# Optimization experiments

Hardware: AMD Instinct MI355X
Metric: run time of the kernel (lower is better)

Reference implementation:

```python
import jax, jax.numpy as jnp
import numpy as np

W_WORKERS = 2
Q_LEN = 16
HIDDEN = 4096
N_HEADS = 32
N_KV = 8
HEAD_DIM = 128
L_SHARED = 8192
L_WORKER = 2048
THETA = 10000.0


def rotate_half(x):
    x1, x2 = jnp.split(x, 2, axis=-1)
    return jnp.concatenate((-x2, x1), axis=-1)


def rope_cos_sin(pos):
    # pos: int array [...]; returns cos,sin of shape [..., HEAD_DIM] (HF convention: freqs duplicated)
    inv = 1.0 / (THETA ** (jnp.arange(0, HEAD_DIM, 2, dtype=jnp.float32) / HEAD_DIM))
    ang = pos[..., None].astype(jnp.float32) * inv
    emb = jnp.concatenate((ang, ang), axis=-1)
    return jnp.cos(emb), jnp.sin(emb)


def setup_inputs() -> dict:
    key = jax.random.key(0)
    ks = jax.random.split(key, 16)
    std = 0.02
    # new keys are appended at positions L_WORKER..L_WORKER+Q-1 of each worker's own segment
    pos_new = jnp.broadcast_to(L_WORKER + jnp.arange(Q_LEN), (W_WORKERS, Q_LEN))
    cos_new, sin_new = rope_cos_sin(pos_new)
    return {
        'hidden_states': jax.random.normal(ks[0], (W_WORKERS, Q_LEN, HIDDEN), jnp.float32),
        'Wq': jax.random.normal(ks[1], (N_HEADS * HEAD_DIM, HIDDEN), jnp.float32) * std,
        'bq': jnp.zeros((N_HEADS * HEAD_DIM,), jnp.float32),
        'Wk': jax.random.normal(ks[2], (N_KV * HEAD_DIM, HIDDEN), jnp.float32) * std,
        'bk': jnp.zeros((N_KV * HEAD_DIM,), jnp.float32),
        'Wv': jax.random.normal(ks[3], (N_KV * HEAD_DIM, HIDDEN), jnp.float32) * std,
        'bv': jnp.zeros((N_KV * HEAD_DIM,), jnp.float32),
        'Wo': jax.random.normal(ks[4], (HIDDEN, N_HEADS * HEAD_DIM), jnp.float32) * std,
        'seg_shared_k': jax.random.normal(ks[5], (N_KV, L_SHARED, HEAD_DIM), jnp.float32),
        'seg_shared_v': jax.random.normal(ks[6], (N_KV, L_SHARED, HEAD_DIM), jnp.float32),
        'w0_k': jax.random.normal(ks[7], (N_KV, L_WORKER, HEAD_DIM), jnp.float32),
        'w0_v': jax.random.normal(ks[8], (N_KV, L_WORKER, HEAD_DIM), jnp.float32),
        'w1_k': jax.random.normal(ks[9], (N_KV, L_WORKER, HEAD_DIM), jnp.float32),
        'w1_v': jax.random.normal(ks[10], (N_KV, L_WORKER, HEAD_DIM), jnp.float32),
        'cos_new': cos_new,
        'sin_new': sin_new,
    }


def reference(hidden_states, Wq, bq, Wk, bk, Wv, bv, Wo,
              seg_shared_k, seg_shared_v, w0_k, w0_v, w1_k, w1_v,
              cos_new, sin_new):
    W, Q, _ = hidden_states.shape
    scale = HEAD_DIM ** -0.5
    # projections -> [W, n_heads, Q, D]
    q = (hidden_states @ Wq.T + bq).reshape(W, Q, N_HEADS, HEAD_DIM).transpose(0, 2, 1, 3)
    k_new = (hidden_states @ Wk.T + bk).reshape(W, Q, N_KV, HEAD_DIM).transpose(0, 2, 1, 3)
    v_new = (hidden_states @ Wv.T + bv).reshape(W, Q, N_KV, HEAD_DIM).transpose(0, 2, 1, 3)
    # rope new keys (unsqueeze_dim=1: broadcast over kv heads)
    c, s = cos_new[:, None], sin_new[:, None]
    k_new = k_new * c + rotate_half(k_new) * s
    # cache update: segment 0 = shared prompt, segment 1/2 = worker 0/1 own cache (grows by Q)
    keys = [seg_shared_k,
            jnp.concatenate([w0_k, k_new[0]], axis=1),
            jnp.concatenate([w1_k, k_new[1]], axis=1)]
    values = [seg_shared_v,
              jnp.concatenate([w0_v, v_new[0]], axis=1),
              jnp.concatenate([w1_v, v_new[1]], axis=1)]
    frag_lens = [L_SHARED, L_WORKER + Q, L_WORKER + Q]
    # worker w's view: [shared, other worker's cache, own cache]
    orders = [[0, 2, 1], [0, 1, 2]]
    loc = np.zeros((3, W_WORKERS, Q), dtype=np.int32)
    for w, order in enumerate(orders):
        pos = 0
        for seg in reversed(order):
            pos += frag_lens[seg]
            loc[seg, w] = np.arange(pos - Q, pos)
    loc = jnp.asarray(loc)  # [S, W, Q]
    cos_q, sin_q = rope_cos_sin(loc)  # [S, W, Q, D]
    # hogwild_rope: queries rotated per (segment, worker) location -> [S, W, H, Q, D]
    rq = q[None] * cos_q[:, :, None] + rotate_half(q)[None] * sin_q[:, :, None]
    rep = N_HEADS // N_KV
    scores, v_parts = [], []
    for seg in range(3):
        k_s = jnp.repeat(keys[seg], rep, axis=0)  # GQA expand [H, L_s, D]
        sc = jnp.einsum('whqd,hld->whql', rq[seg], k_s) * scale
        mask = jnp.arange(frag_lens[seg])[None, None, None, :] <= loc[seg][:, None, :, None]
        scores.append(jnp.where(mask, sc, jnp.finfo(sc.dtype).min))
        v_parts.append(jnp.repeat(values[seg], rep, axis=0))
    scores = jnp.concatenate(scores, axis=-1)        # [W, H, Q, Ltot] joint softmax over fragments
    probs = jax.nn.softmax(scores, axis=-1)
    v_all = jnp.concatenate(v_parts, axis=1)         # [H, Ltot, D]
    attn = jnp.einsum('whql,hld->whqd', probs, v_all)
    out = attn.transpose(0, 2, 1, 3).reshape(W, Q, N_HEADS * HEAD_DIM) @ Wo.T
    return out
```

## Files before the change

### kernel.cpp

```cpp
#include <hip/hip_runtime.h>
#include <hip/hip_fp16.h>
#include <cstdint>
#include <cstddef>

#define QL 16
#define LSH 8192
#define LWK 2048
#define SCALE 0.08838834764831845f

typedef __attribute__((ext_vector_type(8))) short short8;
typedef __attribute__((ext_vector_type(4))) float f32x4;
typedef __attribute__((ext_vector_type(8))) unsigned short ushort8v;

__device__ __forceinline__ unsigned short f2bf(float f) {
  unsigned int u = __float_as_uint(f);
  u += 0x7fffu + ((u >> 16) & 1u);
  return (unsigned short)(u >> 16);
}
__device__ __forceinline__ float bf2f(unsigned short b) {
  return __uint_as_float(((unsigned int)b) << 16);
}

__global__ __launch_bounds__(256) void k_cast(
    const float* __restrict__ in, unsigned short* __restrict__ outp, int n4)
{
  int i = blockIdx.x * 256 + threadIdx.x;
  if (i < n4) {
    float4 v = ((const float4*)in)[i];
    ushort4 p; p.x = f2bf(v.x); p.y = f2bf(v.y); p.z = f2bf(v.z); p.w = f2bf(v.w);
    ((ushort4*)outp)[i] = p;
  }
}

__global__ __launch_bounds__(512) void k_gemm3(
    const unsigned short* __restrict__ Xbf,
    const float* __restrict__ W0, const float* __restrict__ W1, const float* __restrict__ W2,
    const float* __restrict__ b0, const float* __restrict__ b1, const float* __restrict__ b2,
    float* __restrict__ out, int Ntot)
{
  __shared__ float Red[8][512];
  const int n0 = blockIdx.x * 16;
  const float* W; const float* bias; int row0;
  if (n0 < 4096)      { W = W0; bias = b0; row0 = n0; }
  else if (n0 < 5120) { W = W1; bias = b1; row0 = n0 - 4096; }
  else                { W = W2; bias = b2; row0 = n0 - 5120; }
  const int t = threadIdx.x;
  const int w_id = t >> 6;
  const int lane = t & 63;
  const int l15 = lane & 15;
  const int quad = lane >> 4;
  const int kbase = w_id * 512;

  const float* wp = W + (size_t)(row0 + l15) * 4096 + kbase + quad * 8;
  const unsigned short* xp0 = Xbf + (size_t)l15 * 4096 + kbase + quad * 8;
  const unsigned short* xp1 = xp0 + (size_t)16 * 4096;

  f32x4 C0 = {0.f,0.f,0.f,0.f}, C1 = {0.f,0.f,0.f,0.f};

  float4 wa = *(const float4*)(wp);
  float4 wb = *(const float4*)(wp + 4);
  short8 a0 = *(const short8*)(xp0);
  short8 a1 = *(const short8*)(xp1);

#pragma unroll
  for (int s = 0; s < 16; ++s) {
    float4 nwa, nwb; short8 na0, na1;
    if (s < 15) {
      nwa = *(const float4*)(wp + (s + 1) * 32);
      nwb = *(const float4*)(wp + (s + 1) * 32 + 4);
      na0 = *(const short8*)(xp0 + (s + 1) * 32);
      na1 = *(const short8*)(xp1 + (s + 1) * 32);
    }
    short8 bfr;
    bfr[0] = (short)f2bf(wa.x); bfr[1] = (short)f2bf(wa.y);
    bfr[2] = (short)f2bf(wa.z); bfr[3] = (short)f2bf(wa.w);
    bfr[4] = (short)f2bf(wb.x); bfr[5] = (short)f2bf(wb.y);
    bfr[6] = (short)f2bf(wb.z); bfr[7] = (short)f2bf(wb.w);
    C0 = __builtin_amdgcn_mfma_f32_16x16x32_bf16(a0, bfr, C0, 0, 0, 0);
    C1 = __builtin_amdgcn_mfma_f32_16x16x32_bf16(a1, bfr, C1, 0, 0, 0);
    wa = nwa; wb = nwb; a0 = na0; a1 = na1;
  }
#pragma unroll
  for (int i = 0; i < 4; ++i) {
    Red[w_id][(quad * 4 + i) * 16 + l15] = C0[i];
    Red[w_id][(16 + quad * 4 + i) * 16 + l15] = C1[i];
  }
  __syncthreads();
  {
    int m = t >> 4, n = t & 15;
    float s = 0.f;
#pragma unroll
    for (int w = 0; w < 8; ++w) s += Red[w][t];
    if (bias) s += bias[row0 + n];
    out[(size_t)m * Ntot + n0 + n] = s;
  }
}

__global__ __launch_bounds__(256) void k_rope(
    const float* __restrict__ qkv,
    const float* __restrict__ cosn, const float* __restrict__ sinn,
    unsigned short* __restrict__ rq, unsigned short* __restrict__ knew,
    unsigned short* __restrict__ vnew)
{
  const int g = blockIdx.x * 256 + threadIdx.x;
  const float LOGTH = 9.210340371976184f;
  if (g < 393216) {
    int d = g & 127, q = (g >> 7) & 15, head = (g >> 11) & 31, w = (g >> 16) & 1, var = g >> 17;
    int tok = w * 16 + q;
    int col = head * 128 + d;
    float val = qkv[(size_t)tok * 6144 + col];
    float rot = (d < 64) ? -qkv[(size_t)tok * 6144 + col + 64]
                         :  qkv[(size_t)tok * 6144 + col - 64];
    int pos = (var == 0 ? 12304 : (var == 1 ? 4112 : 2048)) + q;
    int i = d & 63;
    float inv = expf(-(float)i * (LOGTH / 64.0f));
    float ang = (float)pos * inv;
    float c = cosf(ang), s = sinf(ang);
    rq[g] = f2bf((val * c + rot * s) * SCALE);
  } else {
    int g2 = g - 393216;
    if (g2 < 65536) {
      int isv = (g2 >= 32768);
      if (isv) g2 -= 32768;
      int d = g2 & 127, q = (g2 >> 7) & 15, h = (g2 >> 11) & 7, w = (g2 >> 14) & 1;
      int tok = w * 16 + q;
      if (isv) {
        vnew[g2] = f2bf(qkv[(size_t)tok * 6144 + 5120 + h * 128 + d]);
      } else {
        int col = 4096 + h * 128 + d;
        float val = qkv[(size_t)tok * 6144 + col];
        float rot = (d < 64) ? -qkv[(size_t)tok * 6144 + col + 64]
                             :  qkv[(size_t)tok * 6144 + col - 64];
        float c = cosn[tok * 128 + d], s = sinn[tok * 128 + d];
        knew[g2] = f2bf(val * c + rot * s);
      }
    }
  }
}

__global__ __launch_bounds__(256, 2) void k_attn(
    const float* __restrict__ shk, const float* __restrict__ shv,
    const float* __restrict__ w0k, const float* __restrict__ w0v,
    const float* __restrict__ w1k, const float* __restrict__ w1v,
    const unsigned short* __restrict__ rq,
    const unsigned short* __restrict__ knew, const unsigned short* __restrict__ vnew,
    __half* __restrict__ accP, float* __restrict__ lP)
{
  __shared__ alignas(16) unsigned short Ks[64 * 136];
  __shared__ alignas(16) unsigned short Vts[128 * 72];
  __shared__ alignas(16) unsigned short Plds[4 * 32 * 72];

  const int h = blockIdx.x / 50;
  const int cidx = blockIdx.x % 50;
  int kind, k0, nk; bool is_new;
  if (cidx < 32)      { kind = 0; k0 = cidx * 256; nk = 256; is_new = false; }
  else if (cidx < 41) { int c = cidx - 32; kind = 1; k0 = c * 256; nk = (c == 8) ? 16 : 256; is_new = (c == 8); }
  else                { int c = cidx - 41; kind = 2; k0 = c * 256; nk = (c == 8) ? 16 : 256; is_new = (c == 8); }

  const int t = threadIdx.x;
  const int w_id = t >> 6;
  const int lane = t & 63;
  const int l15 = lane & 15;
  const int quad = lane >> 4;
  const int worker = w_id >> 1;
  const int headpair = w_id & 1;
  const int tg = t >> 7;
  const int dv = t & 127;
  const int rbase = t >> 5;
  const int doff = (t & 31) * 4;

  int var; bool causal;
  if (kind == 0)      { var = 0; causal = false; }
  else if (kind == 1) { var = (worker == 0) ? 2 : 1; causal = (worker == 0); }
  else                { var = (worker == 1) ? 2 : 1; causal = (worker == 1); }

  const float* Ksrc = (kind == 0) ? (shk + (size_t)h * LSH * 128)
                     : (kind == 1) ? (w0k + (size_t)h * LWK * 128)
                                   : (w1k + (size_t)h * LWK * 128);
  const float* Vsrc = (kind == 0) ? (shv + (size_t)h * LSH * 128)
                     : (kind == 1) ? (w0v + (size_t)h * LWK * 128)
                                   : (w1v + (size_t)h * LWK * 128);
  const int wseg = (kind == 2) ? 1 : 0;
  const unsigned short* knsrc = knew + ((size_t)wseg * 8 + h) * 16 * 128;
  const unsigned short* vnsrc = vnew + ((size_t)wseg * 8 + h) * 16 * 128;

  short8 arq[2][4];
#pragma unroll
  for (int mt = 0; mt < 2; ++mt) {
    int head = h * 4 + headpair * 2 + mt;
    const unsigned short* base =
        rq + ((((size_t)var * 2 + worker) * 32 + head) * 16 + l15) * 128 + quad * 8;
#pragma unroll
    for (int ks = 0; ks < 4; ++ks) arq[mt][ks] = *(const short8*)(base + ks * 32);
  }

  float lrow[2][4];
  f32x4 acc[2][8];
#pragma unroll
  for (int mt = 0; mt < 2; ++mt)
#pragma unroll
    for (int i = 0; i < 4; ++i) lrow[mt][i] = 0.0f;
#pragma unroll
  for (int mt = 0; mt < 2; ++mt)
#pragma unroll
    for (int dt = 0; dt < 8; ++dt) acc[mt][dt] = {0.f,0.f,0.f,0.f};

  float4 kf[8];
  float  vf[32];

  auto load_tile = [&](int st) {
    const int kb = k0 + st * 64;
    if (!is_new) {
#pragma unroll
      for (int rd = 0; rd < 8; ++rd)
        kf[rd] = *(const float4*)(Ksrc + (size_t)(kb + rd * 8 + rbase) * 128 + doff);
#pragma unroll
      for (int g = 0; g < 4; ++g)
#pragma unroll
        for (int i = 0; i < 8; ++i)
          vf[g * 8 + i] = Vsrc[(size_t)(kb + (tg + g * 2) * 8 + i) * 128 + dv];
    } else {
#pragma unroll
      for (int rd = 0; rd < 8; ++rd) {
        ushort4 p = *(const ushort4*)(knsrc + (size_t)((rd * 8 + rbase) & 15) * 128 + doff);
        kf[rd].x = bf2f(p.x); kf[rd].y = bf2f(p.y);
        kf[rd].z = bf2f(p.z); kf[rd].w = bf2f(p.w);
      }
#pragma unroll
      for (int g = 0; g < 4; ++g)
#pragma unroll
        for (int i = 0; i < 8; ++i)
          vf[g * 8 + i] = bf2f(vnsrc[(size_t)(((tg + g * 2) * 8 + i) & 15) * 128 + dv]);
    }
  };

  const int nst = (nk + 63) >> 6;
  load_tile(0);

  for (int st = 0; st < nst; ++st) {
    __syncthreads();
#pragma unroll
    for (int rd = 0; rd < 8; ++rd) {
      ushort4 p; p.x = f2bf(kf[rd].x); p.y = f2bf(kf[rd].y);
      p.z = f2bf(kf[rd].z); p.w = f2bf(kf[rd].w);
      *(ushort4*)(&Ks[(rd * 8 + rbase) * 136 + doff]) = p;
    }
#pragma unroll
    for (int g = 0; g < 4; ++g) {
      ushort8v p;
#pragma unroll
      for (int i = 0; i < 8; ++i) p[i] = f2bf(vf[g * 8 + i]);
      *(ushort8v*)(&Vts[dv * 72 + (tg + g * 2) * 8]) = p;
    }
    __syncthreads();
    if (st + 1 < nst) load_tile(st + 1);

#pragma unroll
    for (int mt = 0; mt < 2; ++mt) {
      f32x4 S[4];
#pragma unroll
      for (int nt = 0; nt < 4; ++nt) S[nt] = {0.f,0.f,0.f,0.f};
#pragma unroll
      for (int ks = 0; ks < 4; ++ks)
#pragma unroll
        for (int nt = 0; nt < 4; ++nt) {
          short8 bfr = *(const short8*)(&Ks[(nt * 16 + l15) * 136 + ks * 32 + quad * 8]);
          S[nt] = __builtin_amdgcn_mfma_f32_16x16x32_bf16(arq[mt][ks], bfr, S[nt], 0, 0, 0);
        }
      if (is_new) {
#pragma unroll
        for (int nt = 0; nt < 4; ++nt) {
          int loc = st * 64 + nt * 16 + l15;
          bool kval = (loc < nk);
#pragma unroll
          for (int i = 0; i < 4; ++i)
            if (!kval || (causal && loc > (quad * 4 + i))) S[nt][i] = -3.0e38f;
        }
      }
      float rs[4] = {0.f, 0.f, 0.f, 0.f};
#pragma unroll
      for (int nt = 0; nt < 4; ++nt)
#pragma unroll
        for (int i = 0; i < 4; ++i) {
          float p = expf(fminf(S[nt][i], 60.0f));
          S[nt][i] = p;
          rs[i] += p;
        }
#pragma unroll
      for (int nt = 0; nt < 4; ++nt)
#pragma unroll
        for (int i = 0; i < 4; ++i)
          Plds[w_id * (32 * 72) + (mt * 16 + quad * 4 + i) * 72 + nt * 16 + l15] =
              f2bf(S[nt][i]);
#pragma unroll
      for (int off = 1; off < 16; off <<= 1)
#pragma unroll
        for (int i = 0; i < 4; ++i) rs[i] += __shfl_xor(rs[i], off, 64);
#pragma unroll
      for (int i = 0; i < 4; ++i) lrow[mt][i] += rs[i];
    }
    short8 ap[2][2];
#pragma unroll
    for (int mt = 0; mt < 2; ++mt)
#pragma unroll
      for (int ks2 = 0; ks2 < 2; ++ks2)
        ap[mt][ks2] = *(const short8*)(
            &Plds[w_id * (32 * 72) + (mt * 16 + l15) * 72 + ks2 * 32 + quad * 8]);
#pragma unroll
    for (int dt = 0; dt < 8; ++dt)
#pragma unroll
      for (int ks2 = 0; ks2 < 2; ++ks2) {
        short8 bfr = *(const short8*)(&Vts[(dt * 16 + l15) * 72 + ks2 * 32 + quad * 8]);
        acc[0][dt] = __builtin_amdgcn_mfma_f32_16x16x32_bf16(ap[0][ks2], bfr, acc[0][dt], 0, 0, 0);
        acc[1][dt] = __builtin_amdgcn_mfma_f32_16x16x32_bf16(ap[1][ks2], bfr, acc[1][dt], 0, 0, 0);
      }
  }

  __half* accB = accP + (size_t)blockIdx.x * 128 * 128;
#pragma unroll
  for (int mt = 0; mt < 2; ++mt)
#pragma unroll
    for (int dt = 0; dt < 8; ++dt)
#pragma unroll
      for (int i = 0; i < 4; ++i) {
        int row = w_id * 32 + mt * 16 + quad * 4 + i;
        int d = dt * 16 + l15;
        accB[row * 128 + d] = __float2half(acc[mt][dt][i]);
      }
  if (l15 == 0) {
#pragma unroll
    for (int mt = 0; mt < 2; ++mt)
#pragma unroll
      for (int i = 0; i < 4; ++i) {
        int row = w_id * 32 + mt * 16 + quad * 4 + i;
        lP[(size_t)blockIdx.x * 128 + row] = lrow[mt][i];
      }
  }
}

__global__ __launch_bounds__(128) void k_combine(
    const __half* __restrict__ accP, const float* __restrict__ lP,
    unsigned short* __restrict__ attnX)
{
  __shared__ float sl[50];
  const int h = blockIdx.x >> 7;
  const int r = blockIdx.x & 127;
  const int d = threadIdx.x;
  if (d < 50) sl[d] = lP[(size_t)(h * 50 + d) * 128 + r];
  __syncthreads();
  float L = 0.0f, A = 0.0f;
#pragma unroll
  for (int c = 0; c < 50; ++c) L += sl[c];
#pragma unroll
  for (int cc = 0; cc < 50; cc += 10) {
    float p[10];
#pragma unroll
    for (int i = 0; i < 10; ++i)
      p[i] = __half2float(accP[((size_t)(h * 50 + cc + i) * 128 + r) * 128 + d]);
#pragma unroll
    for (int i = 0; i < 10; ++i) A += p[i];
  }
  int workerv = r >> 6, headpairv = (r >> 5) & 1, mtv = (r >> 4) & 1, q = r & 15;
  int head = h * 4 + headpairv * 2 + mtv;
  attnX[(size_t)(workerv * 16 + q) * 4096 + head * 128 + d] = f2bf(A / L);
}

extern "C" void kernel_launch(void* const* d_in, const int* in_sizes, int n_in,
                              void* d_out, int out_size, void* d_ws, size_t ws_size,
                              hipStream_t stream)
{
  const float* hs   = (const float*)d_in[0];
  const float* Wq   = (const float*)d_in[1];
  const float* bq   = (const float*)d_in[2];
  const float* Wk   = (const float*)d_in[3];
  const float* bk   = (const float*)d_in[4];
  const float* Wv   = (const float*)d_in[5];
  const float* bv   = (const float*)d_in[6];
  const float* Wo   = (const float*)d_in[7];
  const float* shk  = (const float*)d_in[8];
  const float* shv  = (const float*)d_in[9];
  const float* w0k  = (const float*)d_in[10];
  const float* w0v  = (const float*)d_in[11];
  const float* w1k  = (const float*)d_in[12];
  const float* w1v  = (const float*)d_in[13];
  const float* cosn = (const float*)d_in[14];
  const float* sinn = (const float*)d_in[15];
  float* out = (float*)d_out;

  char* ws = (char*)d_ws;
  float*          qkv    = (float*)(ws + 0);
  unsigned short* rq     = (unsigned short*)(ws + 786432);
  unsigned short* knew   = (unsigned short*)(ws + 1572864);
  unsigned short* vnew   = (unsigned short*)(ws + 1638400);
  unsigned short* hsbf   = (unsigned short*)(ws + 1703936);
  unsigned short* attnXb = (unsigned short*)(ws + 1966080);
  float*          lP     = (float*)(ws + 2228224);
  __half*         accP   = (__half*)(ws + 2433024);

  k_cast<<<128, 256, 0, stream>>>(hs, hsbf, 32768);
  k_gemm3<<<384, 512, 0, stream>>>(hsbf, Wq, Wk, Wv, bq, bk, bv, qkv, 6144);
  k_rope<<<1792, 256, 0, stream>>>(qkv, cosn, sinn, rq, knew, vnew);
  k_attn<<<400, 256, 0, stream>>>(shk, shv, w0k, w0v, w1k, w1v, rq, knew, vnew, accP, lP);
  k_combine<<<1024, 128, 0, stream>>>(accP, lP, attnXb);
  k_gemm3<<<256, 512, 0, stream>>>(attnXb, Wo, Wo, Wo, nullptr, nullptr, nullptr, out, 4096);
}
```

Before: 308.0 us.

## Split-K GEMMs with LDS-staged weights and keep attention probabilities in registers

The QKV and output projection GEMMs are restructured into a split-K form. Each block handles half of K and stages its fp32 weight rows into LDS with global_load_lds, then writes a partial result. A separate add kernel, or the rope kernel for QKV, sums the two partials. Attention now computes S transposed (K as the A operand), so each lane's probabilities can feed a 16x16x16 bf16 MFMA directly, with no LDS round-trip and a cheaper row-sum reduction. The cost is an extra kernel launch, extra partial-sum traffic, and reliance on the mfma 16x16x16 builtin being available.

```diff
diff --git a/kernel.cpp b/kernel.cpp
--- a/kernel.cpp
+++ b/kernel.cpp
@@ -9,8 +9,15 @@
 #define SCALE 0.08838834764831845f
 
 typedef __attribute__((ext_vector_type(8))) short short8;
+typedef __attribute__((ext_vector_type(4))) short short4v;
 typedef __attribute__((ext_vector_type(4))) float f32x4;
 typedef __attribute__((ext_vector_type(8))) unsigned short ushort8v;
+
+#if defined(__has_builtin)
+#if __has_builtin(__builtin_amdgcn_mfma_f32_16x16x16bf16_1k)
+#define HAVE_MFMA16 1
+#endif
+#endif
 
 __device__ __forceinline__ unsigned short f2bf(float f) {
   unsigned int u = __float_as_uint(f);
@@ -19,6 +26,12 @@
 }
 __device__ __forceinline__ float bf2f(unsigned short b) {
   return __uint_as_float(((unsigned int)b) << 16);
+}
+
+__device__ __forceinline__ void gload_lds16(const float* g, float* lds) {
+  __builtin_amdgcn_global_load_lds(
+      (const __attribute__((address_space(1))) void*)g,
+      (__attribute__((address_space(3))) void*)lds, 16, 0, 0);
 }
 
 __global__ __launch_bounds__(256) void k_cast(
@@ -32,14 +45,16 @@
   }
 }
 
-__global__ __launch_bounds__(512) void k_gemm3(
+__global__ __launch_bounds__(256) void k_gemm4(
     const unsigned short* __restrict__ Xbf,
     const float* __restrict__ W0, const float* __restrict__ W1, const float* __restrict__ W2,
     const float* __restrict__ b0, const float* __restrict__ b1, const float* __restrict__ b2,
-    float* __restrict__ out, int Ntot)
-{
-  __shared__ float Red[8][512];
-  const int n0 = blockIdx.x * 16;
+    float* __restrict__ outA, float* __restrict__ outB, int Ntot)
+{
+  __shared__ float Ws[16 * 516];
+  const int bx = blockIdx.x;
+  const int n0 = (bx >> 1) * 16;
+  const int khalf = bx & 1;
   const float* W; const float* bias; int row0;
   if (n0 < 4096)      { W = W0; bias = b0; row0 = n0; }
   else if (n0 < 5120) { W = W1; bias = b1; row0 = n0 - 4096; }
@@ -49,55 +64,70 @@
   const int lane = t & 63;
   const int l15 = lane & 15;
   const int quad = lane >> 4;
-  const int kbase = w_id * 512;
-
-  const float* wp = W + (size_t)(row0 + l15) * 4096 + kbase + quad * 8;
-  const unsigned short* xp0 = Xbf + (size_t)l15 * 4096 + kbase + quad * 8;
-  const unsigned short* xp1 = xp0 + (size_t)16 * 4096;
+  const int cb0 = khalf * 2048;
 
   f32x4 C0 = {0.f,0.f,0.f,0.f}, C1 = {0.f,0.f,0.f,0.f};
 
-  float4 wa = *(const float4*)(wp);
-  float4 wb = *(const float4*)(wp + 4);
-  short8 a0 = *(const short8*)(xp0);
-  short8 a1 = *(const short8*)(xp1);
-
-#pragma unroll
-  for (int s = 0; s < 16; ++s) {
-    float4 nwa, nwb; short8 na0, na1;
-    if (s < 15) {
-      nwa = *(const float4*)(wp + (s + 1) * 32);
-      nwb = *(const float4*)(wp + (s + 1) * 32 + 4);
-      na0 = *(const short8*)(xp0 + (s + 1) * 32);
-      na1 = *(const short8*)(xp1 + (s + 1) * 32);
-    }
-    short8 bfr;
-    bfr[0] = (short)f2bf(wa.x); bfr[1] = (short)f2bf(wa.y);
-    bfr[2] = (short)f2bf(wa.z); bfr[3] = (short)f2bf(wa.w);
-    bfr[4] = (short)f2bf(wb.x); bfr[5] = (short)f2bf(wb.y);
-    bfr[6] = (short)f2bf(wb.z); bfr[7] = (short)f2bf(wb.w);
-    C0 = __builtin_amdgcn_mfma_f32_16x16x32_bf16(a0, bfr, C0, 0, 0, 0);
-    C1 = __builtin_amdgcn_mfma_f32_16x16x32_bf16(a1, bfr, C1, 0, 0, 0);
-    wa = nwa; wb = nwb; a0 = na0; a1 = na1;
-  }
+  for (int c = 0; c < 4; ++c) {
+    const int cbase = cb0 + c * 512;
+    __syncthreads();
+#pragma unroll
+    for (int i = 0; i < 8; ++i) {
+      int idx = w_id * 8 + i;
+      int r = idx >> 1, hh = idx & 1;
+      const float* g = W + (size_t)(row0 + r) * 4096 + cbase + hh * 256 + lane * 4;
+      gload_lds16(g, &Ws[r * 516 + hh * 256]);
+    }
+    __syncthreads();
+    const int wk = w_id * 128;
+#pragma unroll
+    for (int ks = 0; ks < 4; ++ks) {
+      int ko = wk + ks * 32 + quad * 8;
+      f32x4 wlo = *(const f32x4*)(&Ws[l15 * 516 + ko]);
+      f32x4 whi = *(const f32x4*)(&Ws[l15 * 516 + ko + 4]);
+      short8 bfr;
+      bfr[0] = (short)f2bf(wlo[0]); bfr[1] = (short)f2bf(wlo[1]);
+      bfr[2] = (short)f2bf(wlo[2]); bfr[3] = (short)f2bf(wlo[3]);
+      bfr[4] = (short)f2bf(whi[0]); bfr[5] = (short)f2bf(whi[1]);
+      bfr[6] = (short)f2bf(whi[2]); bfr[7] = (short)f2bf(whi[3]);
+      short8 a0 = *(const short8*)(Xbf + (size_t)l15 * 4096 + cbase + ko);
+      short8 a1 = *(const short8*)(Xbf + (size_t)(16 + l15) * 4096 + cbase + ko);
+      C0 = __builtin_amdgcn_mfma_f32_16x16x32_bf16(a0, bfr, C0, 0, 0, 0);
+      C1 = __builtin_amdgcn_mfma_f32_16x16x32_bf16(a1, bfr, C1, 0, 0, 0);
+    }
+  }
+  __syncthreads();
+  float* Red = Ws;
 #pragma unroll
   for (int i = 0; i < 4; ++i) {
-    Red[w_id][(quad * 4 + i) * 16 + l15] = C0[i];
-    Red[w_id][(16 + quad * 4 + i) * 16 + l15] = C1[i];
+    Red[w_id * 512 + (quad * 4 + i) * 16 + l15] = C0[i];
+    Red[w_id * 512 + 256 + (quad * 4 + i) * 16 + l15] = C1[i];
   }
   __syncthreads();
-  {
-    int m = t >> 4, n = t & 15;
-    float s = 0.f;
-#pragma unroll
-    for (int w = 0; w < 8; ++w) s += Red[w][t];
-    if (bias) s += bias[row0 + n];
-    out[(size_t)m * Ntot + n0 + n] = s;
+  float* dst = khalf ? outB : outA;
+#pragma unroll
+  for (int e = t; e < 512; e += 256) {
+    float s = Red[e] + Red[512 + e] + Red[1024 + e] + Red[1536 + e];
+    int m = e >> 4, n = e & 15;
+    if (khalf == 0 && bias) s += bias[row0 + n];
+    dst[(size_t)m * Ntot + n0 + n] = s;
+  }
+}
+
+__global__ __launch_bounds__(256) void k_add(
+    const float* __restrict__ A, const float* __restrict__ B,
+    float* __restrict__ o, int n4)
+{
+  int i = blockIdx.x * 256 + threadIdx.x;
+  if (i < n4) {
+    float4 a = ((const float4*)A)[i], b = ((const float4*)B)[i];
+    float4 r; r.x = a.x + b.x; r.y = a.y + b.y; r.z = a.z + b.z; r.w = a.w + b.w;
+    ((float4*)o)[i] = r;
   }
 }
 
 __global__ __launch_bounds__(256) void k_rope(
-    const float* __restrict__ qkv,
+    const float* __restrict__ qA, const float* __restrict__ qB,
     const float* __restrict__ cosn, const float* __restrict__ sinn,
     unsigned short* __restrict__ rq, unsigned short* __restrict__ knew,
     unsigned short* __restrict__ vnew)
@@ -108,9 +138,11 @@
     int d = g & 127, q = (g >> 7) & 15, head = (g >> 11) & 31, w = (g >> 16) & 1, var = g >> 17;
     int tok = w * 16 + q;
     int col = head * 128 + d;
-    float val = qkv[(size_t)tok * 6144 + col];
-    float rot = (d < 64) ? -qkv[(size_t)tok * 6144 + col + 64]
-                         :  qkv[(size_t)tok * 6144 + col - 64];
+    size_t ix = (size_t)tok * 6144 + col;
+    float val = qA[ix] + qB[ix];
+    size_t ir = (d < 64) ? ix + 64 : ix - 64;
+    float rot = qA[ir] + qB[ir];
+    if (d < 64) rot = -rot;
     int pos = (var == 0 ? 12304 : (var == 1 ? 4112 : 2048)) + q;
     int i = d & 63;
     float inv = expf(-(float)i * (LOGTH / 64.0f));
@@ -125,12 +157,14 @@
       int d = g2 & 127, q = (g2 >> 7) & 15, h = (g2 >> 11) & 7, w = (g2 >> 14) & 1;
       int tok = w * 16 + q;
       if (isv) {
-        vnew[g2] = f2bf(qkv[(size_t)tok * 6144 + 5120 + h * 128 + d]);
+        size_t ix = (size_t)tok * 6144 + 5120 + h * 128 + d;
+        vnew[g2] = f2bf(qA[ix] + qB[ix]);
       } else {
-        int col = 4096 + h * 128 + d;
-        float val = qkv[(size_t)tok * 6144 + col];
-        float rot = (d < 64) ? -qkv[(size_t)tok * 6144 + col + 64]
-                             :  qkv[(size_t)tok * 6144 + col - 64];
+        size_t ix = (size_t)tok * 6144 + 4096 + h * 128 + d;
+        float val = qA[ix] + qB[ix];
+        size_t ir = (d < 64) ? ix + 64 : ix - 64;
+        float rot = qA[ir] + qB[ir];
+        if (d < 64) rot = -rot;
         float c = cosn[tok * 128 + d], s = sinn[tok * 128 + d];
         knew[g2] = f2bf(val * c + rot * s);
       }
@@ -148,7 +182,9 @@
 {
   __shared__ alignas(16) unsigned short Ks[64 * 136];
   __shared__ alignas(16) unsigned short Vts[128 * 72];
+#ifndef HAVE_MFMA16
   __shared__ alignas(16) unsigned short Plds[4 * 32 * 72];
+#endif
 
   const int h = blockIdx.x / 50;
   const int cidx = blockIdx.x % 50;
@@ -194,12 +230,8 @@
     for (int ks = 0; ks < 4; ++ks) arq[mt][ks] = *(const short8*)(base + ks * 32);
   }
 
-  float lrow[2][4];
+  float lrow[2] = {0.f, 0.f};
   f32x4 acc[2][8];
-#pragma unroll
-  for (int mt = 0; mt < 2; ++mt)
-#pragma unroll
-    for (int i = 0; i < 4; ++i) lrow[mt][i] = 0.0f;
 #pragma unroll
   for (int mt = 0; mt < 2; ++mt)
 #pragma unroll
@@ -255,6 +287,9 @@
     __syncthreads();
     if (st + 1 < nst) load_tile(st + 1);
 
+#ifdef HAVE_MFMA16
+    short4v pv[2][4];
+#endif
 #pragma unroll
     for (int mt = 0; mt < 2; ++mt) {
       f32x4 S[4];
@@ -264,41 +299,57 @@
       for (int ks = 0; ks < 4; ++ks)
 #pragma unroll
         for (int nt = 0; nt < 4; ++nt) {
-          short8 bfr = *(const short8*)(&Ks[(nt * 16 + l15) * 136 + ks * 32 + quad * 8]);
-          S[nt] = __builtin_amdgcn_mfma_f32_16x16x32_bf16(arq[mt][ks], bfr, S[nt], 0, 0, 0);
+          short8 kfr = *(const short8*)(&Ks[(nt * 16 + l15) * 136 + ks * 32 + quad * 8]);
+          S[nt] = __builtin_amdgcn_mfma_f32_16x16x32_bf16(kfr, arq[mt][ks], S[nt], 0, 0, 0);
         }
       if (is_new) {
 #pragma unroll
-        for (int nt = 0; nt < 4; ++nt) {
-          int loc = st * 64 + nt * 16 + l15;
-          bool kval = (loc < nk);
-#pragma unroll
-          for (int i = 0; i < 4; ++i)
-            if (!kval || (causal && loc > (quad * 4 + i))) S[nt][i] = -3.0e38f;
+        for (int nt = 0; nt < 4; ++nt)
+#pragma unroll
+          for (int i = 0; i < 4; ++i) {
+            int loc = st * 64 + nt * 16 + quad * 4 + i;
+            if (loc >= nk || (causal && loc > l15)) S[nt][i] = -3.0e38f;
+          }
+      }
+      float rs = 0.0f;
+#pragma unroll
+      for (int nt = 0; nt < 4; ++nt)
+#pragma unroll
+        for (int i = 0; i < 4; ++i) {
+          float p = __expf(fminf(S[nt][i], 60.0f));
+          S[nt][i] = p;
+          rs += p;
         }
-      }
-      float rs[4] = {0.f, 0.f, 0.f, 0.f};
+#ifdef HAVE_MFMA16
+#pragma unroll
+      for (int nt = 0; nt < 4; ++nt) {
+        short4v pp;
+        pp[0] = (short)f2bf(S[nt][0]); pp[1] = (short)f2bf(S[nt][1]);
+        pp[2] = (short)f2bf(S[nt][2]); pp[3] = (short)f2bf(S[nt][3]);
+        pv[mt][nt] = pp;
+      }
+#else
 #pragma unroll
       for (int nt = 0; nt < 4; ++nt)
 #pragma unroll
-        for (int i = 0; i < 4; ++i) {
-          float p = expf(fminf(S[nt][i], 60.0f));
-          S[nt][i] = p;
-          rs[i] += p;
-        }
-#pragma unroll
-      for (int nt = 0; nt < 4; ++nt)
-#pragma unroll
         for (int i = 0; i < 4; ++i)
-          Plds[w_id * (32 * 72) + (mt * 16 + quad * 4 + i) * 72 + nt * 16 + l15] =
+          Plds[w_id * (32 * 72) + (mt * 16 + l15) * 72 + nt * 16 + quad * 4 + i] =
               f2bf(S[nt][i]);
-#pragma unroll
-      for (int off = 1; off < 16; off <<= 1)
-#pragma unroll
-        for (int i = 0; i < 4; ++i) rs[i] += __shfl_xor(rs[i], off, 64);
-#pragma unroll
-      for (int i = 0; i < 4; ++i) lrow[mt][i] += rs[i];
-    }
+#endif
+      rs += __shfl_xor(rs, 16, 64);
+      rs += __shfl_xor(rs, 32, 64);
+      lrow[mt] += rs;
+    }
+#ifdef HAVE_MFMA16
+#pragma unroll
+    for (int dt = 0; dt < 8; ++dt)
+#pragma unroll
+      for (int kc = 0; kc < 4; ++kc) {
+        short4v vfr = *(const short4v*)(&Vts[(dt * 16 + l15) * 72 + kc * 16 + quad * 4]);
+        acc[0][dt] = __builtin_amdgcn_mfma_f32_16x16x16bf16_1k(pv[0][kc], vfr, acc[0][dt], 0, 0, 0);
+        acc[1][dt] = __builtin_amdgcn_mfma_f32_16x16x16bf16_1k(pv[1][kc], vfr, acc[1][dt], 0, 0, 0);
+      }
+#else
     short8 ap[2][2];
 #pragma unroll
     for (int mt = 0; mt < 2; ++mt)
@@ -310,10 +361,11 @@
     for (int dt = 0; dt < 8; ++dt)
 #pragma unroll
       for (int ks2 = 0; ks2 < 2; ++ks2) {
-        short8 bfr = *(const short8*)(&Vts[(dt * 16 + l15) * 72 + ks2 * 32 + quad * 8]);
-        acc[0][dt] = __builtin_amdgcn_mfma_f32_16x16x32_bf16(ap[0][ks2], bfr, acc[0][dt], 0, 0, 0);
-        acc[1][dt] = __builtin_amdgcn_mfma_f32_16x16x32_bf16(ap[1][ks2], bfr, acc[1][dt], 0, 0, 0);
-      }
+        short8 vfr = *(const short8*)(&Vts[(dt * 16 + l15) * 72 + ks2 * 32 + quad * 8]);
+        acc[0][dt] = __builtin_amdgcn_mfma_f32_16x16x32_bf16(ap[0][ks2], vfr, acc[0][dt], 0, 0, 0);
+        acc[1][dt] = __builtin_amdgcn_mfma_f32_16x16x32_bf16(ap[1][ks2], vfr, acc[1][dt], 0, 0, 0);
+      }
+#endif
   }
 
   __half* accB = accP + (size_t)blockIdx.x * 128 * 128;
@@ -327,14 +379,12 @@
         int d = dt * 16 + l15;
         accB[row * 128 + d] = __float2half(acc[mt][dt][i]);
       }
-  if (l15 == 0) {
-#pragma unroll
-    for (int mt = 0; mt < 2; ++mt)
-#pragma unroll
-      for (int i = 0; i < 4; ++i) {
-        int row = w_id * 32 + mt * 16 + quad * 4 + i;
-        lP[(size_t)blockIdx.x * 128 + row] = lrow[mt][i];
-      }
+  if (quad == 0) {
+#pragma unroll
+    for (int mt = 0; mt < 2; ++mt) {
+      int row = w_id * 32 + mt * 16 + l15;
+      lP[(size_t)blockIdx.x * 128 + row] = lrow[mt];
+    }
   }
 }
 
@@ -388,7 +438,7 @@
   float* out = (float*)d_out;
 
   char* ws = (char*)d_ws;
-  float*          qkv    = (float*)(ws + 0);
+  float*          qkvA   = (float*)(ws + 0);
   unsigned short* rq     = (unsigned short*)(ws + 786432);
   unsigned short* knew   = (unsigned short*)(ws + 1572864);
   unsigned short* vnew   = (unsigned short*)(ws + 1638400);
@@ -396,11 +446,15 @@
   unsigned short* attnXb = (unsigned short*)(ws + 1966080);
   float*          lP     = (float*)(ws + 2228224);
   __half*         accP   = (__half*)(ws + 2433024);
+  float*          qkvB   = (float*)(ws + 15540224);
+  float*          outA   = (float*)(ws + 2433024);
+  float*          outB   = (float*)(ws + 2433024 + 786432);
 
   k_cast<<<128, 256, 0, stream>>>(hs, hsbf, 32768);
-  k_gemm3<<<384, 512, 0, stream>>>(hsbf, Wq, Wk, Wv, bq, bk, bv, qkv, 6144);
-  k_rope<<<1792, 256, 0, stream>>>(qkv, cosn, sinn, rq, knew, vnew);
+  k_gemm4<<<768, 256, 0, stream>>>(hsbf, Wq, Wk, Wv, bq, bk, bv, qkvA, qkvB, 6144);
+  k_rope<<<1792, 256, 0, stream>>>(qkvA, qkvB, cosn, sinn, rq, knew, vnew);
   k_attn<<<400, 256, 0, stream>>>(shk, shv, w0k, w0v, w1k, w1v, rq, knew, vnew, accP, lP);
   k_combine<<<1024, 128, 0, stream>>>(accP, lP, attnXb);
-  k_gemm3<<<256, 512, 0, stream>>>(attnXb, Wo, Wo, Wo, nullptr, nullptr, nullptr, out, 4096);
-}
+  k_gemm4<<<512, 256, 0, stream>>>(attnXb, Wo, Wo, Wo, nullptr, nullptr, nullptr, outA, outB, 4096);
+  k_add<<<192, 256, 0, stream>>>(outA, outB, out, 49152);
+}
```

Measured after the change: 300.8 us. -2.3%, faster.
